# Performance work log

Measured on AMD Instinct MI355X. Metric: run time of the kernel, lower is better.

The kernel has to match this reference:

```python
import jax, jax.numpy as jnp
import numpy as np

HEAD_SIZE = 64

def setup_inputs() -> dict:
    key = jax.random.key(0)
    ks = jax.random.split(key, 7)
    B, S, H, D = 8, 2048, 768, HEAD_SIZE
    scale = 1.0 / np.sqrt(H)
    return {
        "x": jax.random.normal(ks[0], (B, S, H), dtype=jnp.float32),
        "Wq": jax.random.normal(ks[1], (H, D), dtype=jnp.float32) * scale,
        "bq": jax.random.normal(ks[2], (D,), dtype=jnp.float32) * 0.02,
        "Wk": jax.random.normal(ks[3], (H, D), dtype=jnp.float32) * scale,
        "bk": jax.random.normal(ks[4], (D,), dtype=jnp.float32) * 0.02,
        "Wv": jax.random.normal(ks[5], (H, D), dtype=jnp.float32) * scale,
        "bv": jax.random.normal(ks[6], (D,), dtype=jnp.float32) * 0.02,
    }

def reference(x, Wq, bq, Wk, bk, Wv, bv):
    # Q/K/V projections: [B,S,H] @ [H,D] -> [B,S,D]
    q = x @ Wq + bq
    k = x @ Wk + bk
    v = x @ Wv + bv
    # scaled dot-product scores: [B,S,S]
    scores = jnp.einsum("bsd,btd->bst", q, k) / jnp.sqrt(jnp.float32(HEAD_SIZE))
    probs = jax.nn.softmax(scores, axis=-1)
    # dropout p=0.0 -> identity (matches eval / p=0 training)
    out = jnp.einsum("bst,btd->bsd", probs, v)
    return (out, probs)
```

## Files before the change

### kernel.cpp

```cpp
#include <hip/hip_runtime.h>

#define BB 8
#define SS 2048
#define HH 768
#define DD 64
#define BK 64
#define NK (HH / BK)

typedef short bf16x8 __attribute__((ext_vector_type(8)));
typedef short bf16x4 __attribute__((ext_vector_type(4)));
typedef float f32x16 __attribute__((ext_vector_type(16)));
typedef float f32x4 __attribute__((ext_vector_type(4)));

static __device__ __forceinline__ short f2bf(float f) {
    union { float f; unsigned u; } v; v.f = f;
    unsigned u = v.u + 0x7fff + ((v.u >> 16) & 1);
    return (short)(u >> 16);
}

__global__ __launch_bounds__(256) void w_convert(
    const float* __restrict__ Wq, const float* __restrict__ Wk,
    const float* __restrict__ Wv, short* __restrict__ wT)
{
    __shared__ float ws[64][65];
    const int jj   = blockIdx.x / 12;
    const int h0   = (blockIdx.x % 12) * 64;
    const int tid  = threadIdx.x;
    const float* Wsrc = (jj == 0) ? Wq : (jj == 1 ? Wk : Wv);

    {
        const int hl = tid >> 4;
        const int c4 = tid & 15;
        #pragma unroll
        for (int p = 0; p < 4; ++p) {
            const int h = hl + p * 16;
            float4 v = ((const float4*)(Wsrc + (long)(h0 + h) * DD))[c4];
            ws[h][c4 * 4 + 0] = v.x; ws[h][c4 * 4 + 1] = v.y;
            ws[h][c4 * 4 + 2] = v.z; ws[h][c4 * 4 + 3] = v.w;
        }
    }
    __syncthreads();

    const int d   = tid >> 2;
    const int seg = tid & 3;
    bf16x8 t0, t1;
    #pragma unroll
    for (int m = 0; m < 8; ++m) {
        t0[m] = f2bf(ws[seg * 16 + m][d]);
        t1[m] = f2bf(ws[seg * 16 + 8 + m][d]);
    }
    short* dst = wT + ((long)jj * 64 + d) * HH + h0 + seg * 16;
    *(bf16x8*)dst = t0;
    *(bf16x8*)(dst + 8) = t1;
}

__global__ __launch_bounds__(384) void qkv_mfma(
    const float* __restrict__ x, const short* __restrict__ wT,
    const float* __restrict__ bq, const float* __restrict__ bk,
    const float* __restrict__ bv,
    short* __restrict__ qo, short* __restrict__ ko, short* __restrict__ vT)
{
    __shared__ short xs[2][32][68];

    const int tid  = threadIdx.x;
    const int w    = tid >> 6;
    const int lane = tid & 63;
    const int l31  = lane & 31;
    const int h    = lane >> 5;
    const long row0 = (long)blockIdx.x * 32;

    const int r0 = tid >> 4,        c0 = tid & 15;
    const int r1 = (tid + 384) >> 4, c1 = (tid + 384) & 15;
    const bool has1 = (tid + 384) < 512;

    f32x16 acc;
    #pragma unroll
    for (int i = 0; i < 16; ++i) acc[i] = 0.f;

    float4 st0, st1;
    st0 = ((const float4*)(x + (row0 + r0) * HH))[c0];
    if (has1) st1 = ((const float4*)(x + (row0 + r1) * HH))[c1];
    {
        bf16x4 b0; b0[0]=f2bf(st0.x); b0[1]=f2bf(st0.y); b0[2]=f2bf(st0.z); b0[3]=f2bf(st0.w);
        *(bf16x4*)&xs[0][r0][c0 * 4] = b0;
        if (has1) {
            bf16x4 b1; b1[0]=f2bf(st1.x); b1[1]=f2bf(st1.y); b1[2]=f2bf(st1.z); b1[3]=f2bf(st1.w);
            *(bf16x4*)&xs[0][r1][c1 * 4] = b1;
        }
    }
    __syncthreads();

    const int col = w * 32 + l31;
    const short* wcol = wT + (long)col * HH + h * 8;

    for (int it = 0; it < NK; ++it) {
        const int cur = it & 1;
        if (it < NK - 1) {
            st0 = ((const float4*)(x + (row0 + r0) * HH + (it + 1) * BK))[c0];
            if (has1) st1 = ((const float4*)(x + (row0 + r1) * HH + (it + 1) * BK))[c1];
        }
        #pragma unroll
        for (int kt = 0; kt < 4; ++kt) {
            bf16x8 af = *(const bf16x8*)&xs[cur][l31][kt * 16 + h * 8];
            bf16x8 bf = *(const bf16x8*)(wcol + it * BK + kt * 16);
            acc = __builtin_amdgcn_mfma_f32_32x32x16_bf16(af, bf, acc, 0, 0, 0);
        }
        if (it < NK - 1) {
            __syncthreads();
            bf16x4 b0; b0[0]=f2bf(st0.x); b0[1]=f2bf(st0.y); b0[2]=f2bf(st0.z); b0[3]=f2bf(st0.w);
            *(bf16x4*)&xs[cur ^ 1][r0][c0 * 4] = b0;
            if (has1) {
                bf16x4 b1; b1[0]=f2bf(st1.x); b1[1]=f2bf(st1.y); b1[2]=f2bf(st1.z); b1[3]=f2bf(st1.w);
                *(bf16x4*)&xs[cur ^ 1][r1][c1 * 4] = b1;
            }
            __syncthreads();
        }
    }

    short (*vs)[68] = xs[0];
    const int j = w >> 1;
    const int d = (w & 1) * 32 + l31;
    const float* bptr = (j == 0) ? bq : (j == 1 ? bk : bv);
    const float bias = bptr[d];

    __syncthreads();

    #pragma unroll
    for (int i = 0; i < 16; ++i) {
        const int r = (i & 3) + 8 * (i >> 2) + 4 * h;
        const short val = f2bf(acc[i] + bias);
        if (j == 0)      qo[(row0 + r) * DD + d] = val;
        else if (j == 1) ko[(row0 + r) * DD + d] = val;
        else             vs[r][d] = val;
    }
    __syncthreads();

    if (tid < 256) {
        const int b  = (int)(row0 >> 11);
        const int s0 = (int)(row0 & (SS - 1));
        const int dd  = tid >> 2;
        const int seg = tid & 3;
        bf16x8 t;
        #pragma unroll
        for (int m = 0; m < 8; ++m) t[m] = vs[seg * 8 + m][dd];
        *(bf16x8*)(vT + ((long)b * DD + dd) * SS + s0 + seg * 8) = t;
    }
}

__global__ __launch_bounds__(512) void attn(
    const short* __restrict__ qb, const short* __restrict__ kb,
    const short* __restrict__ vT,
    float* __restrict__ out, float* __restrict__ probs)
{
    __shared__ float pbuf[8][32][34];
    __shared__ float obuf[32][65];
    __shared__ float sumbuf[32][9];

    const int tid  = threadIdx.x;
    const int w    = tid >> 6;
    const int lane = tid & 63;
    const int l31  = lane & 31;
    const int h    = lane >> 5;

    const int b    = blockIdx.x & 7;
    const int row0 = (blockIdx.x >> 3) * 32;
    const int wk0  = w * 256;

    for (int i = tid; i < 32 * 65; i += 512) ((float*)obuf)[i] = 0.f;

    bf16x8 qf[4];
    const short* qrow = qb + ((long)(b * SS + row0 + l31)) * DD + h * 8;
    #pragma unroll
    for (int kt = 0; kt < 4; ++kt) qf[kt] = *(const bf16x8*)(qrow + kt * 16);

    unsigned P8[8][8];
    float s = 0.f;
    const short* kbase = kb + ((long)(b * SS + wk0 + l31)) * DD + h * 8;
    #pragma unroll
    for (int ct = 0; ct < 8; ++ct) {
        f32x16 a;
        #pragma unroll
        for (int i = 0; i < 16; ++i) a[i] = 0.f;
        const short* kp = kbase + (long)ct * 32 * DD;
        #pragma unroll
        for (int kt = 0; kt < 4; ++kt) {
            bf16x8 kf = *(const bf16x8*)(kp + kt * 16);
            a = __builtin_amdgcn_mfma_f32_32x32x16_bf16(kf, qf[kt], a, 0, 0, 0);
        }
        #pragma unroll
        for (int jj = 0; jj < 4; ++jj) {
            const float p0 = __expf(a[4 * jj + 0] * 0.125f);
            const float p1 = __expf(a[4 * jj + 1] * 0.125f);
            const float p2 = __expf(a[4 * jj + 2] * 0.125f);
            const float p3 = __expf(a[4 * jj + 3] * 0.125f);
            s += (p0 + p1) + (p2 + p3);
            unsigned u0, u1;
            asm("v_cvt_pk_bf16_f32 %0, %1, %2" : "=v"(u0) : "v"(p0), "v"(p1));
            asm("v_cvt_pk_bf16_f32 %0, %1, %2" : "=v"(u1) : "v"(p2), "v"(p3));
            P8[ct][2 * jj] = u0; P8[ct][2 * jj + 1] = u1;
        }
    }
    s += __shfl_xor(s, 32);
    if (lane < 32) sumbuf[l31][w] = s;
    __syncthreads();

    float gs = 0.f;
    #pragma unroll
    for (int i = 0; i < 8; ++i) gs += sumbuf[l31][i];
    const float inv = 1.f / gs;

    f32x16 oacc[2];
    #pragma unroll
    for (int i = 0; i < 16; ++i) { oacc[0][i] = 0.f; oacc[1][i] = 0.f; }

    const int qq  = lane >> 3, sg2 = lane & 7;
    const short* vbase = vT + (long)b * DD * SS + wk0 + h * 8;

    #pragma unroll
    for (int ct = 0; ct < 8; ++ct) {
        #pragma unroll
        for (int kk = 0; kk < 2; ++kk) {
            unsigned x0 = P8[ct][4 * kk + 0], x1 = P8[ct][4 * kk + 1];
            unsigned y0 = P8[ct][4 * kk + 2], y1 = P8[ct][4 * kk + 3];
            asm("v_permlane32_swap_b32 %0, %1" : "+v"(x0), "+v"(y0));
            asm("v_permlane32_swap_b32 %0, %1" : "+v"(x1), "+v"(y1));
            union { unsigned u[4]; bf16x8 v; } pf;
            pf.u[0] = x0; pf.u[1] = x1; pf.u[2] = y0; pf.u[3] = y1;
            #pragma unroll
            for (int nt = 0; nt < 2; ++nt) {
                bf16x8 vf = *(const bf16x8*)(vbase + (long)(nt * 32 + l31) * SS
                                             + ct * 32 + kk * 16);
                oacc[nt] = __builtin_amdgcn_mfma_f32_32x32x16_bf16(vf, pf.v, oacc[nt], 0, 0, 0);
            }
        }
        #pragma unroll
        for (int jj = 0; jj < 4; ++jj)
            #pragma unroll
            for (int u = 0; u < 2; ++u) {
                const unsigned pw = P8[ct][2 * jj + u];
                const float fa = __uint_as_float(pw << 16) * inv;
                const float fb = __uint_as_float(pw & 0xffff0000u) * inv;
                pbuf[w][l31][8 * jj + 4 * h + 2 * u + 0] = fa;
                pbuf[w][l31][8 * jj + 4 * h + 2 * u + 1] = fb;
            }
        #pragma unroll
        for (int jj = 0; jj < 4; ++jj) {
            const int q = qq + 8 * jj;
            float2 a2 = *(float2*)&pbuf[w][q][sg2 * 4];
            float2 b2 = *(float2*)&pbuf[w][q][sg2 * 4 + 2];
            f32x4 o4;
            o4[0] = a2.x; o4[1] = a2.y; o4[2] = b2.x; o4[3] = b2.y;
            __builtin_nontemporal_store(o4,
                (f32x4*)(probs + ((long)(b * SS + row0 + q)) * SS + wk0 + ct * 32 + sg2 * 4));
        }
    }

    #pragma unroll
    for (int nt = 0; nt < 2; ++nt)
        #pragma unroll
        for (int i = 0; i < 16; ++i) {
            const int d = nt * 32 + (i & 3) + 8 * (i >> 2) + 4 * h;
            atomicAdd(&obuf[l31][d], oacc[nt][i] * inv);
        }
    __syncthreads();

    const int q   = tid >> 4;
    const int seg = tid & 15;
    float4 val = make_float4(obuf[q][seg * 4 + 0], obuf[q][seg * 4 + 1],
                             obuf[q][seg * 4 + 2], obuf[q][seg * 4 + 3]);
    *(float4*)(out + ((long)(b * SS + row0 + q)) * DD + seg * 4) = val;
}

extern "C" void kernel_launch(void* const* d_in, const int* in_sizes, int n_in,
                              void* d_out, int out_size, void* d_ws, size_t ws_size,
                              hipStream_t stream) {
    const float* x  = (const float*)d_in[0];
    const float* Wq = (const float*)d_in[1];
    const float* bq = (const float*)d_in[2];
    const float* Wk = (const float*)d_in[3];
    const float* bk = (const float*)d_in[4];
    const float* Wv = (const float*)d_in[5];
    const float* bv = (const float*)d_in[6];

    float* out   = (float*)d_out;
    float* probs = (float*)d_out + (long)BB * SS * DD;

    short* q  = (short*)d_ws;
    short* k  = q + (long)BB * SS * DD;
    short* vT = k + (long)BB * SS * DD;
    short* wT = vT + (long)BB * SS * DD;

    w_convert<<<36, 256, 0, stream>>>(Wq, Wk, Wv, wT);
    qkv_mfma<<<(BB * SS) / 32, 384, 0, stream>>>(x, wT, bq, bk, bv, q, k, vT);
    attn<<<BB * (SS / 32), 512, 0, stream>>>(q, k, vT, out, probs);
}
```

Measured before the change: 115.7 us.

## Switch attention to 16x16 MFMA tiles with permuted K rows for direct probs stores

The attention kernel moves from 32x32x16 to 16x16x32 MFMA with 16 query rows per block, doubling the grid. K rows are loaded in a permuted order so each lane's score fragment maps to 8 contiguous key columns. This lets probs be written straight from registers with two 16-byte stores, removing the LDS transpose buffer and the permlane swaps. It also uses exp2 with a folded constant and starts the PV MFMAs before the block-wide sum sync, at the cost of more blocks reloading K/V and half the rows per block.

```diff
diff --git a/kernel.cpp b/kernel.cpp
--- a/kernel.cpp
+++ b/kernel.cpp
@@ -11,6 +11,8 @@
 typedef short bf16x4 __attribute__((ext_vector_type(4)));
 typedef float f32x16 __attribute__((ext_vector_type(16)));
 typedef float f32x4 __attribute__((ext_vector_type(4)));
+
+#define EXPC 0.18033688011112042f
 
 static __device__ __forceinline__ short f2bf(float f) {
     union { float f; unsigned u; } v; v.f = f;
@@ -152,123 +154,111 @@
     const short* __restrict__ vT,
     float* __restrict__ out, float* __restrict__ probs)
 {
-    __shared__ float pbuf[8][32][34];
-    __shared__ float obuf[32][65];
-    __shared__ float sumbuf[32][9];
+    __shared__ float obuf[16][65];
+    __shared__ float sumbuf[16][17];
 
     const int tid  = threadIdx.x;
     const int w    = tid >> 6;
     const int lane = tid & 63;
-    const int l31  = lane & 31;
-    const int h    = lane >> 5;
+    const int l15  = lane & 15;
+    const int g    = (lane >> 4) & 3;
 
     const int b    = blockIdx.x & 7;
-    const int row0 = (blockIdx.x >> 3) * 32;
+    const int row0 = (blockIdx.x >> 3) * 16;
     const int wk0  = w * 256;
 
-    for (int i = tid; i < 32 * 65; i += 512) ((float*)obuf)[i] = 0.f;
-
-    bf16x8 qf[4];
-    const short* qrow = qb + ((long)(b * SS + row0 + l31)) * DD + h * 8;
-    #pragma unroll
-    for (int kt = 0; kt < 4; ++kt) qf[kt] = *(const bf16x8*)(qrow + kt * 16);
-
-    unsigned P8[8][8];
+    for (int i = tid; i < 16 * 65; i += 512) ((float*)obuf)[i] = 0.f;
+
+    const short* qrow = qb + ((long)(b * SS + row0 + l15)) * DD + g * 8;
+    const bf16x8 qf0 = *(const bf16x8*)(qrow);
+    const bf16x8 qf1 = *(const bf16x8*)(qrow + 32);
+
+    unsigned P8[8][4];
     float s = 0.f;
-    const short* kbase = kb + ((long)(b * SS + wk0 + l31)) * DD + h * 8;
-    #pragma unroll
-    for (int ct = 0; ct < 8; ++ct) {
-        f32x16 a;
-        #pragma unroll
-        for (int i = 0; i < 16; ++i) a[i] = 0.f;
-        const short* kp = kbase + (long)ct * 32 * DD;
-        #pragma unroll
-        for (int kt = 0; kt < 4; ++kt) {
-            bf16x8 kf = *(const bf16x8*)(kp + kt * 16);
-            a = __builtin_amdgcn_mfma_f32_32x32x16_bf16(kf, qf[kt], a, 0, 0, 0);
-        }
-        #pragma unroll
-        for (int jj = 0; jj < 4; ++jj) {
-            const float p0 = __expf(a[4 * jj + 0] * 0.125f);
-            const float p1 = __expf(a[4 * jj + 1] * 0.125f);
-            const float p2 = __expf(a[4 * jj + 2] * 0.125f);
-            const float p3 = __expf(a[4 * jj + 3] * 0.125f);
+    const int krow = 8 * (l15 >> 2) + (l15 & 3);
+    const short* kbase = kb + ((long)(b * SS + wk0 + krow)) * DD + g * 8;
+    #pragma unroll
+    for (int wd = 0; wd < 8; ++wd) {
+        #pragma unroll
+        for (int t = 0; t < 2; ++t) {
+            const short* kp = kbase + (long)(wd * 32 + 4 * t) * DD;
+            f32x4 a = {0.f, 0.f, 0.f, 0.f};
+            a = __builtin_amdgcn_mfma_f32_16x16x32_bf16(*(const bf16x8*)kp, qf0, a, 0, 0, 0);
+            a = __builtin_amdgcn_mfma_f32_16x16x32_bf16(*(const bf16x8*)(kp + 32), qf1, a, 0, 0, 0);
+            const float p0 = __builtin_amdgcn_exp2f(a[0] * EXPC);
+            const float p1 = __builtin_amdgcn_exp2f(a[1] * EXPC);
+            const float p2 = __builtin_amdgcn_exp2f(a[2] * EXPC);
+            const float p3 = __builtin_amdgcn_exp2f(a[3] * EXPC);
             s += (p0 + p1) + (p2 + p3);
             unsigned u0, u1;
             asm("v_cvt_pk_bf16_f32 %0, %1, %2" : "=v"(u0) : "v"(p0), "v"(p1));
             asm("v_cvt_pk_bf16_f32 %0, %1, %2" : "=v"(u1) : "v"(p2), "v"(p3));
-            P8[ct][2 * jj] = u0; P8[ct][2 * jj + 1] = u1;
-        }
-    }
+            P8[wd][2 * t] = u0; P8[wd][2 * t + 1] = u1;
+        }
+    }
+    s += __shfl_xor(s, 16);
     s += __shfl_xor(s, 32);
-    if (lane < 32) sumbuf[l31][w] = s;
+    if (lane < 16) sumbuf[l15][w] = s;
+
+    f32x4 oacc[4];
+    #pragma unroll
+    for (int nt = 0; nt < 4; ++nt) { oacc[nt][0]=0.f; oacc[nt][1]=0.f; oacc[nt][2]=0.f; oacc[nt][3]=0.f; }
+
+    const short* vbase = vT + (long)b * DD * SS + wk0 + g * 8;
+    #pragma unroll
+    for (int wd = 0; wd < 8; ++wd) {
+        union { unsigned u[4]; bf16x8 v; } pf;
+        pf.u[0] = P8[wd][0]; pf.u[1] = P8[wd][1];
+        pf.u[2] = P8[wd][2]; pf.u[3] = P8[wd][3];
+        #pragma unroll
+        for (int nt = 0; nt < 4; ++nt) {
+            const bf16x8 vf = *(const bf16x8*)(vbase + (long)(nt * 16 + l15) * SS + wd * 32);
+            oacc[nt] = __builtin_amdgcn_mfma_f32_16x16x32_bf16(vf, pf.v, oacc[nt], 0, 0, 0);
+        }
+    }
     __syncthreads();
 
     float gs = 0.f;
     #pragma unroll
-    for (int i = 0; i < 8; ++i) gs += sumbuf[l31][i];
+    for (int i = 0; i < 8; ++i) gs += sumbuf[l15][i];
     const float inv = 1.f / gs;
 
-    f32x16 oacc[2];
-    #pragma unroll
-    for (int i = 0; i < 16; ++i) { oacc[0][i] = 0.f; oacc[1][i] = 0.f; }
-
-    const int qq  = lane >> 3, sg2 = lane & 7;
-    const short* vbase = vT + (long)b * DD * SS + wk0 + h * 8;
-
-    #pragma unroll
-    for (int ct = 0; ct < 8; ++ct) {
-        #pragma unroll
-        for (int kk = 0; kk < 2; ++kk) {
-            unsigned x0 = P8[ct][4 * kk + 0], x1 = P8[ct][4 * kk + 1];
-            unsigned y0 = P8[ct][4 * kk + 2], y1 = P8[ct][4 * kk + 3];
-            asm("v_permlane32_swap_b32 %0, %1" : "+v"(x0), "+v"(y0));
-            asm("v_permlane32_swap_b32 %0, %1" : "+v"(x1), "+v"(y1));
-            union { unsigned u[4]; bf16x8 v; } pf;
-            pf.u[0] = x0; pf.u[1] = x1; pf.u[2] = y0; pf.u[3] = y1;
-            #pragma unroll
-            for (int nt = 0; nt < 2; ++nt) {
-                bf16x8 vf = *(const bf16x8*)(vbase + (long)(nt * 32 + l31) * SS
-                                             + ct * 32 + kk * 16);
-                oacc[nt] = __builtin_amdgcn_mfma_f32_32x32x16_bf16(vf, pf.v, oacc[nt], 0, 0, 0);
-            }
-        }
-        #pragma unroll
-        for (int jj = 0; jj < 4; ++jj)
-            #pragma unroll
-            for (int u = 0; u < 2; ++u) {
-                const unsigned pw = P8[ct][2 * jj + u];
-                const float fa = __uint_as_float(pw << 16) * inv;
-                const float fb = __uint_as_float(pw & 0xffff0000u) * inv;
-                pbuf[w][l31][8 * jj + 4 * h + 2 * u + 0] = fa;
-                pbuf[w][l31][8 * jj + 4 * h + 2 * u + 1] = fb;
-            }
-        #pragma unroll
-        for (int jj = 0; jj < 4; ++jj) {
-            const int q = qq + 8 * jj;
-            float2 a2 = *(float2*)&pbuf[w][q][sg2 * 4];
-            float2 b2 = *(float2*)&pbuf[w][q][sg2 * 4 + 2];
-            f32x4 o4;
-            o4[0] = a2.x; o4[1] = a2.y; o4[2] = b2.x; o4[3] = b2.y;
-            __builtin_nontemporal_store(o4,
-                (f32x4*)(probs + ((long)(b * SS + row0 + q)) * SS + wk0 + ct * 32 + sg2 * 4));
-        }
-    }
-
-    #pragma unroll
-    for (int nt = 0; nt < 2; ++nt)
-        #pragma unroll
-        for (int i = 0; i < 16; ++i) {
-            const int d = nt * 32 + (i & 3) + 8 * (i >> 2) + 4 * h;
-            atomicAdd(&obuf[l31][d], oacc[nt][i] * inv);
-        }
-    __syncthreads();
-
-    const int q   = tid >> 4;
-    const int seg = tid & 15;
-    float4 val = make_float4(obuf[q][seg * 4 + 0], obuf[q][seg * 4 + 1],
-                             obuf[q][seg * 4 + 2], obuf[q][seg * 4 + 3]);
-    *(float4*)(out + ((long)(b * SS + row0 + q)) * DD + seg * 4) = val;
+    float* prow = probs + ((long)(b * SS + row0 + l15)) * SS + wk0 + 8 * g;
+    #pragma unroll
+    for (int wd = 0; wd < 8; ++wd) {
+        f32x4 o0, o1;
+        {
+            const unsigned a0 = P8[wd][0], a1 = P8[wd][1];
+            o0[0] = __uint_as_float(a0 << 16) * inv;
+            o0[1] = __uint_as_float(a0 & 0xffff0000u) * inv;
+            o0[2] = __uint_as_float(a1 << 16) * inv;
+            o0[3] = __uint_as_float(a1 & 0xffff0000u) * inv;
+        }
+        {
+            const unsigned a2 = P8[wd][2], a3 = P8[wd][3];
+            o1[0] = __uint_as_float(a2 << 16) * inv;
+            o1[1] = __uint_as_float(a2 & 0xffff0000u) * inv;
+            o1[2] = __uint_as_float(a3 << 16) * inv;
+            o1[3] = __uint_as_float(a3 & 0xffff0000u) * inv;
+        }
+        __builtin_nontemporal_store(o0, (f32x4*)(prow + wd * 32));
+        __builtin_nontemporal_store(o1, (f32x4*)(prow + wd * 32 + 4));
+    }
+
+    #pragma unroll
+    for (int nt = 0; nt < 4; ++nt)
+        #pragma unroll
+        for (int r = 0; r < 4; ++r)
+            atomicAdd(&obuf[l15][nt * 16 + 4 * g + r], oacc[nt][r] * inv);
+    __syncthreads();
+
+    if (tid < 256) {
+        const int q  = tid >> 4;
+        const int c4 = tid & 15;
+        float4 val = make_float4(obuf[q][c4 * 4 + 0], obuf[q][c4 * 4 + 1],
+                                 obuf[q][c4 * 4 + 2], obuf[q][c4 * 4 + 3]);
+        *(float4*)(out + ((long)(b * SS + row0 + q)) * DD + c4 * 4) = val;
+    }
 }
 
 extern "C" void kernel_launch(void* const* d_in, const int* in_sizes, int n_in,
@@ -292,5 +282,5 @@
 
     w_convert<<<36, 256, 0, stream>>>(Wq, Wk, Wv, wT);
     qkv_mfma<<<(BB * SS) / 32, 384, 0, stream>>>(x, wT, bq, bk, bv, q, k, vT);
-    attn<<<BB * (SS / 32), 512, 0, stream>>>(q, k, vT, out, probs);
-}
+    attn<<<BB * (SS / 16), 512, 0, stream>>>(q, k, vT, out, probs);
+}
```

Result: slower. 134.7 us (+16.5%).

## Permute K rows so MFMA output feeds PV directly and store probs without LDS

Applied to the files above, without the earlier changes.

Loads K rows in a permuted order (sigma) so the score accumulator layout already matches the B-operand layout of the PV MFMA. This removes the permlane32 swaps and lets the PV product run inside the same loop as the scores. Probs are written straight from registers as float4 stores, dropping the LDS staging buffer and its reads. Exp is computed with exp2 and a folded constant. The cost is that the normalized probs are written after the sum barrier from live P8 registers, and the stores are no longer nontemporal and less coalesced per instruction.

```diff
diff --git a/kernel.cpp b/kernel.cpp
--- a/kernel.cpp
+++ b/kernel.cpp
@@ -12,10 +12,16 @@
 typedef float f32x16 __attribute__((ext_vector_type(16)));
 typedef float f32x4 __attribute__((ext_vector_type(4)));
 
+#define EXPC 0.18033688011112042f
+
 static __device__ __forceinline__ short f2bf(float f) {
     union { float f; unsigned u; } v; v.f = f;
     unsigned u = v.u + 0x7fff + ((v.u >> 16) & 1);
     return (short)(u >> 16);
+}
+
+static __device__ __forceinline__ int sigma(int j) {
+    return (j & 19) | ((j & 4) << 1) | ((j & 8) >> 1);
 }
 
 __global__ __launch_bounds__(256) void w_convert(
@@ -152,7 +158,6 @@
     const short* __restrict__ vT,
     float* __restrict__ out, float* __restrict__ probs)
 {
-    __shared__ float pbuf[8][32][34];
     __shared__ float obuf[32][65];
     __shared__ float sumbuf[32][9];
 
@@ -169,63 +174,48 @@
     for (int i = tid; i < 32 * 65; i += 512) ((float*)obuf)[i] = 0.f;
 
     bf16x8 qf[4];
-    const short* qrow = qb + ((long)(b * SS + row0 + l31)) * DD + h * 8;
+    const short* qrow = qb + ((long)(b * SS) + row0 + l31) * DD + h * 8;
     #pragma unroll
     for (int kt = 0; kt < 4; ++kt) qf[kt] = *(const bf16x8*)(qrow + kt * 16);
 
+    const int sl = sigma(l31);
+    const short* kbase = kb + ((long)(b * SS) + wk0 + sl) * DD + h * 8;
+    const short* vbase = vT + (long)b * DD * SS + wk0 + h * 8;
+
     unsigned P8[8][8];
+    f32x16 oacc[2];
+    #pragma unroll
+    for (int i = 0; i < 16; ++i) { oacc[0][i] = 0.f; oacc[1][i] = 0.f; }
     float s = 0.f;
-    const short* kbase = kb + ((long)(b * SS + wk0 + l31)) * DD + h * 8;
+
     #pragma unroll
     for (int ct = 0; ct < 8; ++ct) {
+        const short* kp = kbase + (long)ct * 32 * DD;
         f32x16 a;
         #pragma unroll
         for (int i = 0; i < 16; ++i) a[i] = 0.f;
-        const short* kp = kbase + (long)ct * 32 * DD;
         #pragma unroll
         for (int kt = 0; kt < 4; ++kt) {
             bf16x8 kf = *(const bf16x8*)(kp + kt * 16);
             a = __builtin_amdgcn_mfma_f32_32x32x16_bf16(kf, qf[kt], a, 0, 0, 0);
         }
         #pragma unroll
-        for (int jj = 0; jj < 4; ++jj) {
-            const float p0 = __expf(a[4 * jj + 0] * 0.125f);
-            const float p1 = __expf(a[4 * jj + 1] * 0.125f);
-            const float p2 = __expf(a[4 * jj + 2] * 0.125f);
-            const float p3 = __expf(a[4 * jj + 3] * 0.125f);
-            s += (p0 + p1) + (p2 + p3);
-            unsigned u0, u1;
-            asm("v_cvt_pk_bf16_f32 %0, %1, %2" : "=v"(u0) : "v"(p0), "v"(p1));
-            asm("v_cvt_pk_bf16_f32 %0, %1, %2" : "=v"(u1) : "v"(p2), "v"(p3));
-            P8[ct][2 * jj] = u0; P8[ct][2 * jj + 1] = u1;
-        }
-    }
-    s += __shfl_xor(s, 32);
-    if (lane < 32) sumbuf[l31][w] = s;
-    __syncthreads();
-
-    float gs = 0.f;
-    #pragma unroll
-    for (int i = 0; i < 8; ++i) gs += sumbuf[l31][i];
-    const float inv = 1.f / gs;
-
-    f32x16 oacc[2];
-    #pragma unroll
-    for (int i = 0; i < 16; ++i) { oacc[0][i] = 0.f; oacc[1][i] = 0.f; }
-
-    const int qq  = lane >> 3, sg2 = lane & 7;
-    const short* vbase = vT + (long)b * DD * SS + wk0 + h * 8;
-
-    #pragma unroll
-    for (int ct = 0; ct < 8; ++ct) {
+        for (int i = 0; i < 16; ++i) {
+            a[i] = __builtin_amdgcn_exp2f(a[i] * EXPC);
+            s += a[i];
+        }
+        #pragma unroll
+        for (int i = 0; i < 8; ++i) {
+            unsigned u;
+            asm("v_cvt_pk_bf16_f32 %0, %1, %2"
+                : "=v"(u) : "v"(a[2 * i]), "v"(a[2 * i + 1]));
+            P8[ct][i] = u;
+        }
         #pragma unroll
         for (int kk = 0; kk < 2; ++kk) {
-            unsigned x0 = P8[ct][4 * kk + 0], x1 = P8[ct][4 * kk + 1];
-            unsigned y0 = P8[ct][4 * kk + 2], y1 = P8[ct][4 * kk + 3];
-            asm("v_permlane32_swap_b32 %0, %1" : "+v"(x0), "+v"(y0));
-            asm("v_permlane32_swap_b32 %0, %1" : "+v"(x1), "+v"(y1));
             union { unsigned u[4]; bf16x8 v; } pf;
-            pf.u[0] = x0; pf.u[1] = x1; pf.u[2] = y0; pf.u[3] = y1;
+            pf.u[0] = P8[ct][4 * kk + 0]; pf.u[1] = P8[ct][4 * kk + 1];
+            pf.u[2] = P8[ct][4 * kk + 2]; pf.u[3] = P8[ct][4 * kk + 3];
             #pragma unroll
             for (int nt = 0; nt < 2; ++nt) {
                 bf16x8 vf = *(const bf16x8*)(vbase + (long)(nt * 32 + l31) * SS
@@ -233,42 +223,75 @@
                 oacc[nt] = __builtin_amdgcn_mfma_f32_32x32x16_bf16(vf, pf.v, oacc[nt], 0, 0, 0);
             }
         }
-        #pragma unroll
-        for (int jj = 0; jj < 4; ++jj)
-            #pragma unroll
-            for (int u = 0; u < 2; ++u) {
-                const unsigned pw = P8[ct][2 * jj + u];
-                const float fa = __uint_as_float(pw << 16) * inv;
-                const float fb = __uint_as_float(pw & 0xffff0000u) * inv;
-                pbuf[w][l31][8 * jj + 4 * h + 2 * u + 0] = fa;
-                pbuf[w][l31][8 * jj + 4 * h + 2 * u + 1] = fb;
-            }
-        #pragma unroll
-        for (int jj = 0; jj < 4; ++jj) {
-            const int q = qq + 8 * jj;
-            float2 a2 = *(float2*)&pbuf[w][q][sg2 * 4];
-            float2 b2 = *(float2*)&pbuf[w][q][sg2 * 4 + 2];
-            f32x4 o4;
-            o4[0] = a2.x; o4[1] = a2.y; o4[2] = b2.x; o4[3] = b2.y;
-            __builtin_nontemporal_store(o4,
-                (f32x4*)(probs + ((long)(b * SS + row0 + q)) * SS + wk0 + ct * 32 + sg2 * 4));
-        }
+    }
+
+    s += __shfl_xor(s, 32);
+    if (lane < 32) sumbuf[l31][w] = s;
+    __syncthreads();
+    float gs = 0.f;
+    #pragma unroll
+    for (int i = 0; i < 8; ++i) gs += sumbuf[l31][i];
+    const float inv = 1.f / gs;
+
+    float* prow = probs + ((long)(b * SS) + row0 + l31) * SS + wk0 + 8 * h;
+    #pragma unroll
+    for (int ct = 0; ct < 8; ++ct) {
+        f32x4 o0, o1, o2, o3;
+        #pragma unroll
+        for (int i = 0; i < 2; ++i) {
+            const unsigned u0 = P8[ct][2 * i + 0], u1 = P8[ct][2 * i + 1];
+            o0[2 * i + 0] = __uint_as_float(u0 << 16) * inv;
+            o0[2 * i + 1] = __uint_as_float(u0 & 0xffff0000u) * inv;
+            o1[2 * i + 0] = __uint_as_float(u1 << 16) * inv;
+            o1[2 * i + 1] = __uint_as_float(u1 & 0xffff0000u) * inv;
+        }
+        #pragma unroll
+        for (int i = 0; i < 2; ++i) {
+            const unsigned u0 = P8[ct][4 + 2 * i], u1 = P8[ct][5 + 2 * i];
+            o2[2 * i + 0] = __uint_as_float(u0 << 16) * inv;
+            o2[2 * i + 1] = __uint_as_float(u0 & 0xffff0000u) * inv;
+            o3[2 * i + 0] = __uint_as_float(u1 << 16) * inv;
+            o3[2 * i + 1] = __uint_as_float(u1 & 0xffff0000u) * inv;
+        }
+        float* pp = prow + ct * 32;
+        f32x4 q0, q1, q2, q3;
+        q0[0] = __uint_as_float(P8[ct][0] << 16) * inv;
+        q0[1] = __uint_as_float(P8[ct][0] & 0xffff0000u) * inv;
+        q0[2] = __uint_as_float(P8[ct][1] << 16) * inv;
+        q0[3] = __uint_as_float(P8[ct][1] & 0xffff0000u) * inv;
+        q1[0] = __uint_as_float(P8[ct][2] << 16) * inv;
+        q1[1] = __uint_as_float(P8[ct][2] & 0xffff0000u) * inv;
+        q1[2] = __uint_as_float(P8[ct][3] << 16) * inv;
+        q1[3] = __uint_as_float(P8[ct][3] & 0xffff0000u) * inv;
+        q2[0] = __uint_as_float(P8[ct][4] << 16) * inv;
+        q2[1] = __uint_as_float(P8[ct][4] & 0xffff0000u) * inv;
+        q2[2] = __uint_as_float(P8[ct][5] << 16) * inv;
+        q2[3] = __uint_as_float(P8[ct][5] & 0xffff0000u) * inv;
+        q3[0] = __uint_as_float(P8[ct][6] << 16) * inv;
+        q3[1] = __uint_as_float(P8[ct][6] & 0xffff0000u) * inv;
+        q3[2] = __uint_as_float(P8[ct][7] << 16) * inv;
+        q3[3] = __uint_as_float(P8[ct][7] & 0xffff0000u) * inv;
+        *(f32x4*)(pp)          = q0;
+        *(f32x4*)(pp + 4)      = q1;
+        *(f32x4*)(pp + 16)     = q2;
+        *(f32x4*)(pp + 16 + 4) = q3;
     }
 
     #pragma unroll
     for (int nt = 0; nt < 2; ++nt)
         #pragma unroll
-        for (int i = 0; i < 16; ++i) {
-            const int d = nt * 32 + (i & 3) + 8 * (i >> 2) + 4 * h;
-            atomicAdd(&obuf[l31][d], oacc[nt][i] * inv);
-        }
-    __syncthreads();
-
-    const int q   = tid >> 4;
-    const int seg = tid & 15;
-    float4 val = make_float4(obuf[q][seg * 4 + 0], obuf[q][seg * 4 + 1],
-                             obuf[q][seg * 4 + 2], obuf[q][seg * 4 + 3]);
-    *(float4*)(out + ((long)(b * SS + row0 + q)) * DD + seg * 4) = val;
+        for (int i = 0; i < 16; ++i)
+            atomicAdd(&obuf[l31][nt * 32 + (i & 3) + 8 * (i >> 2) + 4 * h],
+                      oacc[nt][i] * inv);
+    __syncthreads();
+
+    {
+        const int q   = tid >> 4;
+        const int seg = tid & 15;
+        float4 val = make_float4(obuf[q][seg * 4 + 0], obuf[q][seg * 4 + 1],
+                                 obuf[q][seg * 4 + 2], obuf[q][seg * 4 + 3]);
+        *(float4*)(out + ((long)(b * SS) + row0 + q) * DD + seg * 4) = val;
+    }
 }
 
 extern "C" void kernel_launch(void* const* d_in, const int* in_sizes, int n_in,
```

Result: slower. 123.7 us (+6.9%).
